# Kernel optimization log

Hardware: AMD Instinct MI355X
Metric: run time of the kernel (lower is better)

The kernel has to match this reference:

```python
import jax, jax.numpy as jnp
import numpy as np

B, N, C = 8192, 64, 256  # batch, num_nodes, cells; depth=2


def setup_inputs() -> dict:
    key = jax.random.key(0)
    ks = jax.random.split(key, 9)
    scale1 = 1.0  # fan_in = 1
    scaleC = 1.0 / np.sqrt(C)
    return {
        "Q": jax.random.normal(ks[0], (B, N), dtype=jnp.float32),
        "Y": jax.random.normal(ks[1], (B, N), dtype=jnp.float32),
        # stacked per-node MLP params: Linear(1,C) -> ReLU -> Linear(C,C) -> ReLU -> Linear(C,1)
        "W1": jax.random.normal(ks[2], (N, 1, C), dtype=jnp.float32) * scale1,
        "b1": jax.random.normal(ks[3], (N, C), dtype=jnp.float32) * scale1,
        "W2": jax.random.normal(ks[4], (N, C, C), dtype=jnp.float32) * scaleC,
        "b2": jax.random.normal(ks[5], (N, C), dtype=jnp.float32) * scaleC,
        "W3": jax.random.normal(ks[6], (N, C, 1), dtype=jnp.float32) * scaleC,
        "b3": jax.random.normal(ks[7], (N, 1), dtype=jnp.float32) * scaleC,
        "bias_0": jnp.ones((1, 1), dtype=jnp.float32),
    }


def reference(Q, Y, W1, b1, W2, b2, W3, b3, bias_0):
    s = Q * Y  # [B, N], per-node scalar input s_i = q_i * y_i
    # layer 1: scalar -> C  (W1[n,0,:] broadcast over batch)
    h = jax.nn.relu(s[:, :, None] * W1[None, :, 0, :] + b1[None])  # [B, N, C]
    # layer 2: C -> C, batched over nodes
    h = jax.nn.relu(jnp.einsum("bnc,ncd->bnd", h, W2) + b2[None])  # [B, N, C]
    # layer 3: C -> scalar
    z_i = jnp.einsum("bnc,nc->bn", h, W3[:, :, 0]) + b3[None, :, 0]  # [B, N]
    z_0 = bias_0 - jnp.sum(s, axis=-1, keepdims=True)  # [B, 1]
    z = jnp.concatenate([z_0, z_i], axis=-1)  # [B, N+1]
    z = jax.nn.softmax(z, axis=-1)
    return jax.nn.relu(z)
```

## Files before the change

### kernel.cpp

```cpp
#include <hip/hip_runtime.h>
#include <hip/hip_bf16.h>


typedef unsigned int u32;

__device__ __forceinline__ float row_reduce16(float x) {
    int v;
    v = __builtin_amdgcn_update_dpp(0, __float_as_int(x), 0xB1, 0xF, 0xF, false);
    x += __int_as_float(v);
    v = __builtin_amdgcn_update_dpp(0, __float_as_int(x), 0x4E, 0xF, 0xF, false);
    x += __int_as_float(v);
    v = __builtin_amdgcn_update_dpp(0, __float_as_int(x), 0x124, 0xF, 0xF, false);
    x += __int_as_float(v);
    v = __builtin_amdgcn_update_dpp(0, __float_as_int(x), 0x128, 0xF, 0xF, false);
    x += __int_as_float(v);
    return x;
}

__global__ __launch_bounds__(256) void prep(
    const float* __restrict__ Q, const float* __restrict__ Y,
    const float* __restrict__ W1, const float* __restrict__ b1,
    float* __restrict__ S, float* __restrict__ knots, int* __restrict__ perm)
{
    __shared__ float ts[64][65];
    __shared__ float key[256];
    __shared__ int   idx[256];

    const int blk = blockIdx.x;
    const int tid = threadIdx.x;

    if (blk < 128) {
        const int b0 = blk << 6;
        #pragma unroll
        for (int jj = 0; jj < 16; jj++) {
            int i = tid + (jj << 8);
            int r = i >> 6, c = i & 63;
            ts[r][c] = Q[(size_t)(b0 + r) * 64 + c] * Y[(size_t)(b0 + r) * 64 + c];
        }
        __syncthreads();
        #pragma unroll
        for (int jj = 0; jj < 16; jj++) {
            int i = tid + (jj << 8);
            int nn = i >> 6, bb = i & 63;
            S[((size_t)nn << 13) + b0 + bb] = ts[bb][nn];
        }
    } else {
        const int n = blk - 128;
        {
            float w = W1[n * 256 + tid];
            float b = b1[n * 256 + tid];
            key[tid] = -b / w;
            idx[tid] = tid;
        }
        __syncthreads();
        for (int k = 2; k <= 256; k <<= 1) {
            for (int j = k >> 1; j > 0; j >>= 1) {
                int p = tid ^ j;
                if (p > tid) {
                    float a = key[tid], c = key[p];
                    bool up = ((tid & k) == 0);
                    if (up ? (a > c) : (a < c)) {
                        int ia = idx[tid];
                        key[tid] = c; idx[tid] = idx[p];
                        key[p] = a; idx[p] = ia;
                    }
                }
                __syncthreads();
            }
        }
        knots[n * 256 + tid] = key[tid];
        perm[n * 256 + tid]  = idx[tid];
    }
}

__global__ __launch_bounds__(256) void build_sort(
    const float* __restrict__ W1, const float* __restrict__ b1,
    const float* __restrict__ W2, const float* __restrict__ b2,
    const float* __restrict__ W3, const int* __restrict__ perm,
    const float* __restrict__ S, const float* __restrict__ knots,
    float4* __restrict__ entries, float2* __restrict__ AccP,
    unsigned char* __restrict__ cnt8, uint2* __restrict__ sorted)
{
    __shared__ float  w1s[256], b1s[256], kns[256];
    __shared__ int    pm[256];
    __shared__ float  part[16][16][8];
    __shared__ float2 accL[257];
    __shared__ u32    hist[257];

    const int blk = blockIdx.x;
    const int tid = threadIdx.x;
    const int lane = tid & 63;

    if (blk < 512) {
        const int n    = blk >> 3;
        const int strip= blk & 7;
        const int prl  = tid & 15;
        const int seg  = tid >> 4;
        const int prg  = (strip << 4) + prl;
        const int d0   = prg << 1;
        const int g    = (n << 3) + strip;

        w1s[tid] = W1[n * 256 + tid];
        b1s[tid] = b1[n * 256 + tid];
        kns[tid] = knots[n * 256 + tid];
        pm[tid]  = perm[n * 256 + tid];
        __syncthreads();

        const float w30 = W3[n * 256 + d0];
        const float w31 = W3[n * 256 + d0 + 1];
        const float* W2n = W2 + ((size_t)n << 16);
        float2 vreg[16];

        {
            float ba0 = 0.f, bc0 = 0.f, ba1 = 0.f, bc1 = 0.f;
            float da0 = 0.f, dc0 = 0.f, da1 = 0.f, dc1 = 0.f;
            #pragma unroll
            for (int i = 0; i < 16; ++i) {
                int   kj = pm[(seg << 4) + i];
                float w  = w1s[kj];
                float bb = b1s[kj];
                float2 v = *reinterpret_cast<const float2*>(&W2n[kj * 256 + d0]);
                vreg[i] = v;
                if (w < 0.f) {
                    ba0 = fmaf(v.x, w, ba0); bc0 = fmaf(v.x, bb, bc0);
                    ba1 = fmaf(v.y, w, ba1); bc1 = fmaf(v.y, bb, bc1);
                }
                float aw = fabsf(w);
                float cs = (w > 0.f) ? bb : -bb;
                da0 = fmaf(v.x, aw, da0); dc0 = fmaf(v.x, cs, dc0);
                da1 = fmaf(v.y, aw, da1); dc1 = fmaf(v.y, cs, dc1);
            }
            float* p = part[seg][prl];
            p[0] = ba0; p[1] = bc0; p[2] = ba1; p[3] = bc1;
            p[4] = da0; p[5] = dc0; p[6] = da1; p[7] = dc1;
        }
        __syncthreads();

        if (tid < 16) {
            const int pr = tid;
            float sa0 = 0.f, sc0 = 0.f, sa1 = 0.f, sc1 = 0.f;
            #pragma unroll
            for (int sg = 0; sg < 16; ++sg) {
                const float* p = part[sg][pr];
                sa0 += p[0]; sc0 += p[1]; sa1 += p[2]; sc1 += p[3];
            }
            const int dd = ((strip << 4) + pr) << 1;
            sc0 += b2[n * 256 + dd];
            sc1 += b2[n * 256 + dd + 1];

            float k0 = kns[0];
            float hLo0 = (sa0 != 0.f) ? -sa0 : sc0;
            float hHi0 = fmaf(sa0, k0, sc0);
            float hLo1 = (sa1 != 0.f) ? -sa1 : sc1;
            float hHi1 = fmaf(sa1, k0, sc1);
            bool act0 = hLo0 > 0.f && hHi0 > 0.f, drp0 = hLo0 <= 0.f && hHi0 <= 0.f;
            bool act1 = hLo1 > 0.f && hHi1 > 0.f, drp1 = hLo1 <= 0.f && hHi1 <= 0.f;
            bool cr0 = !act0 && !drp0, cr1 = !act1 && !drp1;
            float As = (act0 ? w30 * sa0 : 0.f) + (act1 ? w31 * sa1 : 0.f);
            float Bs = (act0 ? w30 * sc0 : 0.f) + (act1 ? w31 * sc1 : 0.f);
            As = row_reduce16(As); Bs = row_reduce16(Bs);
            u32 cx = (u32)cr0 + (u32)cr1;
            u32 incl = cx, t;
            t = __shfl_up(incl, 1, 64); if (pr >= 1) incl += t;
            t = __shfl_up(incl, 2, 64); if (pr >= 2) incl += t;
            t = __shfl_up(incl, 4, 64); if (pr >= 4) incl += t;
            t = __shfl_up(incl, 8, 64); if (pr >= 8) incl += t;
            u32 excl = incl - cx;
            u32 tot  = __shfl(incl, 15, 64);
            size_t eb = ((size_t)(n * 257 + 0) * 8 + strip) * 32;
            u32 off = excl;
            if (cr0) { entries[eb + off] = make_float4(sa0, sc0, w30, 0.f); off++; }
            if (cr1) { entries[eb + off] = make_float4(sa1, sc1, w31, 0.f); }
            if (pr == 0) { accL[0] = make_float2(As, Bs); hist[0] = tot; }

            float ra0 = sa0, rc0 = sc0, ra1 = sa1, rc1 = sc1;
            #pragma unroll
            for (int sg = 0; sg < 16; ++sg) {
                float* p = part[sg][pr];
                float t4 = p[4], t5 = p[5], t6 = p[6], t7 = p[7];
                p[0] = ra0; p[1] = rc0; p[2] = ra1; p[3] = rc1;
                ra0 += t4; rc0 += t5; ra1 += t6; rc1 += t7;
            }
        }
        __syncthreads();

        {
            const float* p = part[seg][prl];
            float a0 = p[0], c0 = p[1], a1 = p[2], c1 = p[3];
            #pragma unroll 4
            for (int i = 0; i < 16; ++i) {
                int   j  = (seg << 4) + i;
                int   kj = pm[j];
                float w  = w1s[kj];
                float bb = b1s[kj];
                float2 v = vreg[i];
                float aw = fabsf(w);
                float cs = (w > 0.f) ? bb : -bb;
                a0 = fmaf(v.x, aw, a0); c0 = fmaf(v.x, cs, c0);
                a1 = fmaf(v.y, aw, a1); c1 = fmaf(v.y, cs, c1);

                float lo = kns[j];
                float hLo0 = fmaf(a0, lo, c0), hLo1 = fmaf(a1, lo, c1);
                float hHi0, hHi1;
                if (j < 255) {
                    float hi = kns[j + 1];
                    hHi0 = fmaf(a0, hi, c0); hHi1 = fmaf(a1, hi, c1);
                } else {
                    hHi0 = (a0 != 0.f) ? a0 : c0;
                    hHi1 = (a1 != 0.f) ? a1 : c1;
                }
                bool act0 = hLo0 > 0.f && hHi0 > 0.f, drp0 = hLo0 <= 0.f && hHi0 <= 0.f;
                bool act1 = hLo1 > 0.f && hHi1 > 0.f, drp1 = hLo1 <= 0.f && hHi1 <= 0.f;
                bool cr0 = !act0 && !drp0, cr1 = !act1 && !drp1;
                float As = (act0 ? w30 * a0 : 0.f) + (act1 ? w31 * a1 : 0.f);
                float Bs = (act0 ? w30 * c0 : 0.f) + (act1 ? w31 * c1 : 0.f);
                As = row_reduce16(As); Bs = row_reduce16(Bs);
                u32 cx = (u32)cr0 + (u32)cr1;
                u32 incl = cx, t;
                t = __shfl_up(incl, 1, 64); if (prl >= 1) incl += t;
                t = __shfl_up(incl, 2, 64); if (prl >= 2) incl += t;
                t = __shfl_up(incl, 4, 64); if (prl >= 4) incl += t;
                t = __shfl_up(incl, 8, 64); if (prl >= 8) incl += t;
                u32 excl = incl - cx;
                u32 tot  = __shfl(incl, (lane & ~15) + 15, 64);
                size_t eb = ((size_t)(n * 257 + (j + 1)) * 8 + strip) * 32;
                u32 off = excl;
                if (cr0) { entries[eb + off] = make_float4(a0, c0, w30, 0.f); off++; }
                if (cr1) { entries[eb + off] = make_float4(a1, c1, w31, 0.f); }
                if (prl == 0) {
                    accL[j + 1] = make_float2(As, Bs);
                    hist[j + 1] = tot;
                }
            }
        }
        __syncthreads();

        for (int i = tid; i < 257; i += 256) {
            AccP[(size_t)g * 257 + i] = accL[i];
            cnt8[(size_t)g * 257 + i] = (unsigned char)hist[i];
        }
    } else {
        const int t = blk - 512;
        const int n = t >> 2;
        const int q = t & 3;

        float* kn = w1s;
        kn[tid] = knots[n * 256 + tid];
        hist[tid] = 0;
        if (tid == 0) hist[256] = 0;
        __syncthreads();

        const float* Sn = S + ((size_t)n << 13) + (q << 11);
        float sv[8]; int iv[8];
        #pragma unroll
        for (int j = 0; j < 8; ++j) {
            const float s = Sn[tid + (j << 8)];
            sv[j] = s;
            int I = 0;
            #pragma unroll
            for (int step = 128; step >= 1; step >>= 1)
                if (kn[I + step - 1] < s) I += step;
            if (I < 256 && kn[I] < s) I += 1;
            iv[j] = I;
            atomicAdd(&hist[I], 1u);
        }
        __syncthreads();

        if (tid < 64) {
            int base = tid << 2;
            u32 h0 = hist[base], h1 = hist[base + 1], h2 = hist[base + 2], h3 = hist[base + 3];
            u32 lsum = h0 + h1 + h2 + h3;
            u32 run = lsum;
            #pragma unroll
            for (int off = 1; off < 64; off <<= 1) {
                u32 tt = __shfl_up(run, off, 64);
                if (lane >= off) run += tt;
            }
            u32 excl = run - lsum;
            hist[base]     = excl;
            hist[base + 1] = excl + h0;
            hist[base + 2] = excl + h0 + h1;
            hist[base + 3] = excl + h0 + h1 + h2;
            if (tid == 63) hist[256] = excl + lsum;
        }
        __syncthreads();

        uint2* dst = sorted + ((size_t)n << 13) + (q << 11);
        #pragma unroll
        for (int j = 0; j < 8; ++j) {
            u32 pos = atomicAdd(&hist[iv[j]], 1u);
            u32 bglob = (u32)((q << 11) + tid + (j << 8));
            dst[pos] = make_uint2(__float_as_uint(sv[j]), ((u32)iv[j] << 13) | bglob);
        }
    }
}

__global__ __launch_bounds__(256) void eval_nodes(
    const uint2* __restrict__ sorted, const float4* __restrict__ entries,
    const float2* __restrict__ AccP, const unsigned char* __restrict__ cnt8,
    const float* __restrict__ b3, float* __restrict__ Z)
{
    const int n   = blockIdx.x;
    const int c0  = blockIdx.y << 8;
    const int tid = threadIdx.x;

    const uint2 ent = sorted[((size_t)n << 13) + c0 + tid];
    const float s   = __uint_as_float(ent.x);
    const int   I   = (int)(ent.y >> 13);
    const int   bl  = (int)(ent.y & 8191u);

    const size_t ibase = (size_t)(n * 257 + I) * 8;

    float A = 0.f, B = 0.f, zc = 0.f;
    #pragma unroll
    for (int st = 0; st < 8; ++st) {
        const size_t gi = (size_t)((n << 3) + st) * 257 + I;
        float2 ap = AccP[gi];
        A += ap.x; B += ap.y;
        u32 c = cnt8[gi];
        const float4* ep = entries + ((ibase + st) << 5);
        for (u32 jj = 0; jj < c; ++jj) {
            float4 e = ep[jj];
            zc = fmaf(e.z, fmaxf(fmaf(e.x, s, e.y), 0.f), zc);
        }
    }
    Z[((size_t)n << 13) + bl] = fmaf(A, s, B) + zc + b3[n];
}

__global__ __launch_bounds__(256) void softmax_rows(
    const float* __restrict__ Q, const float* __restrict__ Y,
    const float* __restrict__ Z, const float* __restrict__ bias0,
    float* __restrict__ out)
{
    __shared__ float ts[64][65];
    const int b0   = blockIdx.x << 6;
    const int tid  = threadIdx.x;
    const int lane = tid & 63;
    const int wv   = tid >> 6;

    #pragma unroll
    for (int jj = 0; jj < 16; jj++) {
        int idx = tid + (jj << 8);
        int nn = idx >> 6, bb = idx & 63;
        ts[bb][nn] = Z[((size_t)nn << 13) + b0 + bb];
    }
    __syncthreads();

    const float bias = bias0[0];
    #pragma unroll 2
    for (int r = 0; r < 16; ++r) {
        const int row = (wv << 4) + r;
        const int b   = b0 + row;

        float s = Q[(size_t)b * 64 + lane] * Y[(size_t)b * 64 + lane];
        float ssum = s;
        #pragma unroll
        for (int mask = 32; mask >= 1; mask >>= 1) ssum += __shfl_xor(ssum, mask, 64);
        const float z0 = bias - ssum;

        float zl = ts[row][lane];
        float mx = zl;
        #pragma unroll
        for (int mask = 32; mask >= 1; mask >>= 1) mx = fmaxf(mx, __shfl_xor(mx, mask, 64));
        mx = fmaxf(mx, z0);

        float el = expf(zl - mx);
        float e0 = expf(z0 - mx);
        float den = el;
        #pragma unroll
        for (int mask = 32; mask >= 1; mask >>= 1) den += __shfl_xor(den, mask, 64);
        den += e0;
        const float inv = 1.0f / den;

        out[(size_t)b * 65 + 1 + lane] = el * inv;
        if (lane == 0) out[(size_t)b * 65] = e0 * inv;
    }
}

extern "C" void kernel_launch(void* const* d_in, const int* in_sizes, int n_in,
                              void* d_out, int out_size, void* d_ws, size_t ws_size,
                              hipStream_t stream)
{
    const float* Q     = (const float*)d_in[0];
    const float* Y     = (const float*)d_in[1];
    const float* W1    = (const float*)d_in[2];
    const float* b1    = (const float*)d_in[3];
    const float* W2    = (const float*)d_in[4];
    const float* b2    = (const float*)d_in[5];
    const float* W3    = (const float*)d_in[6];
    const float* b3    = (const float*)d_in[7];
    const float* bias0 = (const float*)d_in[8];
    float* out = (float*)d_out;

    char* ws = (char*)d_ws;
    float4* entries      = (float4*)ws;
    float2* AccP         = (float2*)(ws + 67371008);
    unsigned char* cnt8  = (unsigned char*)(ws + 68423680);
    float* S             = (float*)(ws + 68555264);
    float* Z             = (float*)(ws + 70652416);
    float* knots         = (float*)(ws + 72749568);
    int*   perm          = (int*)  (ws + 72815104);
    uint2* sorted        = (uint2*)(ws + 72880640);

    prep<<<192, 256, 0, stream>>>(Q, Y, W1, b1, S, knots, perm);
    build_sort<<<768, 256, 0, stream>>>(W1, b1, W2, b2, W3, perm, S, knots,
                                        entries, AccP, cnt8, sorted);
    eval_nodes<<<dim3(64, 32), 256, 0, stream>>>(sorted, entries, AccP, cnt8, b3, Z);
    softmax_rows<<<128, 256, 0, stream>>>(Q, Y, Z, bias0, out);
}
```

Before: 55.71 us.

## Move knot binning and sort into eval_nodes as a per-block LDS sort

The bucket-sort of per-batch scalars by knot interval moves out of the build kernel, where it ran as 256 extra blocks writing a global sorted array, into eval_nodes. Each eval block now does the binary search, histogram, scan and scatter in shared memory over its own 256 samples. This removes the global sorted buffer's write and read traffic and drops the build kernel to 512 blocks. In exchange, sorting happens only within each 256-sample chunk, so lanes in a wave share interval indices less often and the entry loops diverge more; eval_nodes also gains LDS work and syncs.

```diff
diff --git a/kernel.cpp b/kernel.cpp
--- a/kernel.cpp
+++ b/kernel.cpp
@@ -73,248 +73,238 @@
     }
 }
 
-__global__ __launch_bounds__(256) void build_sort(
+__global__ __launch_bounds__(256) void build_scan(
     const float* __restrict__ W1, const float* __restrict__ b1,
     const float* __restrict__ W2, const float* __restrict__ b2,
     const float* __restrict__ W3, const int* __restrict__ perm,
-    const float* __restrict__ S, const float* __restrict__ knots,
+    const float* __restrict__ knots,
     float4* __restrict__ entries, float2* __restrict__ AccP,
-    unsigned char* __restrict__ cnt8, uint2* __restrict__ sorted)
+    unsigned char* __restrict__ cnt8)
 {
     __shared__ float  w1s[256], b1s[256], kns[256];
     __shared__ int    pm[256];
     __shared__ float  part[16][16][8];
     __shared__ float2 accL[257];
-    __shared__ u32    hist[257];
-
-    const int blk = blockIdx.x;
-    const int tid = threadIdx.x;
+    __shared__ u32    cntL[257];
+
+    const int tid  = threadIdx.x;
     const int lane = tid & 63;
-
-    if (blk < 512) {
-        const int n    = blk >> 3;
-        const int strip= blk & 7;
-        const int prl  = tid & 15;
-        const int seg  = tid >> 4;
-        const int prg  = (strip << 4) + prl;
-        const int d0   = prg << 1;
-        const int g    = (n << 3) + strip;
-
-        w1s[tid] = W1[n * 256 + tid];
-        b1s[tid] = b1[n * 256 + tid];
-        kns[tid] = knots[n * 256 + tid];
-        pm[tid]  = perm[n * 256 + tid];
-        __syncthreads();
-
-        const float w30 = W3[n * 256 + d0];
-        const float w31 = W3[n * 256 + d0 + 1];
-        const float* W2n = W2 + ((size_t)n << 16);
-        float2 vreg[16];
-
-        {
-            float ba0 = 0.f, bc0 = 0.f, ba1 = 0.f, bc1 = 0.f;
-            float da0 = 0.f, dc0 = 0.f, da1 = 0.f, dc1 = 0.f;
-            #pragma unroll
-            for (int i = 0; i < 16; ++i) {
-                int   kj = pm[(seg << 4) + i];
-                float w  = w1s[kj];
-                float bb = b1s[kj];
-                float2 v = *reinterpret_cast<const float2*>(&W2n[kj * 256 + d0]);
-                vreg[i] = v;
-                if (w < 0.f) {
-                    ba0 = fmaf(v.x, w, ba0); bc0 = fmaf(v.x, bb, bc0);
-                    ba1 = fmaf(v.y, w, ba1); bc1 = fmaf(v.y, bb, bc1);
-                }
-                float aw = fabsf(w);
-                float cs = (w > 0.f) ? bb : -bb;
-                da0 = fmaf(v.x, aw, da0); dc0 = fmaf(v.x, cs, dc0);
-                da1 = fmaf(v.y, aw, da1); dc1 = fmaf(v.y, cs, dc1);
+    const int n    = blockIdx.x >> 3;
+    const int strip= blockIdx.x & 7;
+    const int prl  = tid & 15;
+    const int seg  = tid >> 4;
+    const int d0   = ((strip << 4) + prl) << 1;
+    const int g    = (n << 3) + strip;
+
+    w1s[tid] = W1[n * 256 + tid];
+    b1s[tid] = b1[n * 256 + tid];
+    kns[tid] = knots[n * 256 + tid];
+    pm[tid]  = perm[n * 256 + tid];
+    __syncthreads();
+
+    const float w30 = W3[n * 256 + d0];
+    const float w31 = W3[n * 256 + d0 + 1];
+    const float* W2n = W2 + ((size_t)n << 16);
+    float2 vreg[16];
+
+    {
+        float ba0 = 0.f, bc0 = 0.f, ba1 = 0.f, bc1 = 0.f;
+        float da0 = 0.f, dc0 = 0.f, da1 = 0.f, dc1 = 0.f;
+        #pragma unroll
+        for (int i = 0; i < 16; ++i) {
+            int   kj = pm[(seg << 4) + i];
+            float w  = w1s[kj];
+            float bb = b1s[kj];
+            float2 v = *reinterpret_cast<const float2*>(&W2n[kj * 256 + d0]);
+            vreg[i] = v;
+            if (w < 0.f) {
+                ba0 = fmaf(v.x, w, ba0); bc0 = fmaf(v.x, bb, bc0);
+                ba1 = fmaf(v.y, w, ba1); bc1 = fmaf(v.y, bb, bc1);
             }
-            float* p = part[seg][prl];
-            p[0] = ba0; p[1] = bc0; p[2] = ba1; p[3] = bc1;
-            p[4] = da0; p[5] = dc0; p[6] = da1; p[7] = dc1;
-        }
-        __syncthreads();
-
-        if (tid < 16) {
-            const int pr = tid;
-            float sa0 = 0.f, sc0 = 0.f, sa1 = 0.f, sc1 = 0.f;
-            #pragma unroll
-            for (int sg = 0; sg < 16; ++sg) {
-                const float* p = part[sg][pr];
-                sa0 += p[0]; sc0 += p[1]; sa1 += p[2]; sc1 += p[3];
+            float aw = fabsf(w);
+            float cs = (w > 0.f) ? bb : -bb;
+            da0 = fmaf(v.x, aw, da0); dc0 = fmaf(v.x, cs, dc0);
+            da1 = fmaf(v.y, aw, da1); dc1 = fmaf(v.y, cs, dc1);
+        }
+        float* p = part[seg][prl];
+        p[0] = ba0; p[1] = bc0; p[2] = ba1; p[3] = bc1;
+        p[4] = da0; p[5] = dc0; p[6] = da1; p[7] = dc1;
+    }
+    __syncthreads();
+
+    if (tid < 16) {
+        const int pr = tid;
+        float sa0 = 0.f, sc0 = 0.f, sa1 = 0.f, sc1 = 0.f;
+        #pragma unroll
+        for (int sg = 0; sg < 16; ++sg) {
+            const float* p = part[sg][pr];
+            sa0 += p[0]; sc0 += p[1]; sa1 += p[2]; sc1 += p[3];
+        }
+        const int dd = ((strip << 4) + pr) << 1;
+        sc0 += b2[n * 256 + dd];
+        sc1 += b2[n * 256 + dd + 1];
+
+        float k0 = kns[0];
+        float hLo0 = (sa0 != 0.f) ? -sa0 : sc0;
+        float hHi0 = fmaf(sa0, k0, sc0);
+        float hLo1 = (sa1 != 0.f) ? -sa1 : sc1;
+        float hHi1 = fmaf(sa1, k0, sc1);
+        bool act0 = hLo0 > 0.f && hHi0 > 0.f, drp0 = hLo0 <= 0.f && hHi0 <= 0.f;
+        bool act1 = hLo1 > 0.f && hHi1 > 0.f, drp1 = hLo1 <= 0.f && hHi1 <= 0.f;
+        bool cr0 = !act0 && !drp0, cr1 = !act1 && !drp1;
+        float As = (act0 ? w30 * sa0 : 0.f) + (act1 ? w31 * sa1 : 0.f);
+        float Bs = (act0 ? w30 * sc0 : 0.f) + (act1 ? w31 * sc1 : 0.f);
+        As = row_reduce16(As); Bs = row_reduce16(Bs);
+        u32 cx = (u32)cr0 + (u32)cr1;
+        u32 incl = cx, t;
+        t = __shfl_up(incl, 1, 64); if (pr >= 1) incl += t;
+        t = __shfl_up(incl, 2, 64); if (pr >= 2) incl += t;
+        t = __shfl_up(incl, 4, 64); if (pr >= 4) incl += t;
+        t = __shfl_up(incl, 8, 64); if (pr >= 8) incl += t;
+        u32 excl = incl - cx;
+        u32 tot  = __shfl(incl, 15, 64);
+        size_t eb = ((size_t)(n * 257 + 0) * 8 + strip) * 32;
+        u32 off = excl;
+        if (cr0) { entries[eb + off] = make_float4(sa0, sc0, w30, 0.f); off++; }
+        if (cr1) { entries[eb + off] = make_float4(sa1, sc1, w31, 0.f); }
+        if (pr == 0) { accL[0] = make_float2(As, Bs); cntL[0] = tot; }
+
+        float ra0 = sa0, rc0 = sc0, ra1 = sa1, rc1 = sc1;
+        #pragma unroll
+        for (int sg = 0; sg < 16; ++sg) {
+            float* p = part[sg][pr];
+            float t4 = p[4], t5 = p[5], t6 = p[6], t7 = p[7];
+            p[0] = ra0; p[1] = rc0; p[2] = ra1; p[3] = rc1;
+            ra0 += t4; rc0 += t5; ra1 += t6; rc1 += t7;
+        }
+    }
+    __syncthreads();
+
+    {
+        const float* p = part[seg][prl];
+        float a0 = p[0], c0 = p[1], a1 = p[2], c1 = p[3];
+        #pragma unroll 4
+        for (int i = 0; i < 16; ++i) {
+            int   j  = (seg << 4) + i;
+            int   kj = pm[j];
+            float w  = w1s[kj];
+            float bb = b1s[kj];
+            float2 v = vreg[i];
+            float aw = fabsf(w);
+            float cs = (w > 0.f) ? bb : -bb;
+            a0 = fmaf(v.x, aw, a0); c0 = fmaf(v.x, cs, c0);
+            a1 = fmaf(v.y, aw, a1); c1 = fmaf(v.y, cs, c1);
+
+            float lo = kns[j];
+            float hLo0 = fmaf(a0, lo, c0), hLo1 = fmaf(a1, lo, c1);
+            float hHi0, hHi1;
+            if (j < 255) {
+                float hi = kns[j + 1];
+                hHi0 = fmaf(a0, hi, c0); hHi1 = fmaf(a1, hi, c1);
+            } else {
+                hHi0 = (a0 != 0.f) ? a0 : c0;
+                hHi1 = (a1 != 0.f) ? a1 : c1;
             }
-            const int dd = ((strip << 4) + pr) << 1;
-            sc0 += b2[n * 256 + dd];
-            sc1 += b2[n * 256 + dd + 1];
-
-            float k0 = kns[0];
-            float hLo0 = (sa0 != 0.f) ? -sa0 : sc0;
-            float hHi0 = fmaf(sa0, k0, sc0);
-            float hLo1 = (sa1 != 0.f) ? -sa1 : sc1;
-            float hHi1 = fmaf(sa1, k0, sc1);
             bool act0 = hLo0 > 0.f && hHi0 > 0.f, drp0 = hLo0 <= 0.f && hHi0 <= 0.f;
             bool act1 = hLo1 > 0.f && hHi1 > 0.f, drp1 = hLo1 <= 0.f && hHi1 <= 0.f;
             bool cr0 = !act0 && !drp0, cr1 = !act1 && !drp1;
-            float As = (act0 ? w30 * sa0 : 0.f) + (act1 ? w31 * sa1 : 0.f);
-            float Bs = (act0 ? w30 * sc0 : 0.f) + (act1 ? w31 * sc1 : 0.f);
+            float As = (act0 ? w30 * a0 : 0.f) + (act1 ? w31 * a1 : 0.f);
+            float Bs = (act0 ? w30 * c0 : 0.f) + (act1 ? w31 * c1 : 0.f);
             As = row_reduce16(As); Bs = row_reduce16(Bs);
             u32 cx = (u32)cr0 + (u32)cr1;
             u32 incl = cx, t;
-            t = __shfl_up(incl, 1, 64); if (pr >= 1) incl += t;
-            t = __shfl_up(incl, 2, 64); if (pr >= 2) incl += t;
-            t = __shfl_up(incl, 4, 64); if (pr >= 4) incl += t;
-            t = __shfl_up(incl, 8, 64); if (pr >= 8) incl += t;
+            t = __shfl_up(incl, 1, 64); if (prl >= 1) incl += t;
+            t = __shfl_up(incl, 2, 64); if (prl >= 2) incl += t;
+            t = __shfl_up(incl, 4, 64); if (prl >= 4) incl += t;
+            t = __shfl_up(incl, 8, 64); if (prl >= 8) incl += t;
             u32 excl = incl - cx;
-            u32 tot  = __shfl(incl, 15, 64);
-            size_t eb = ((size_t)(n * 257 + 0) * 8 + strip) * 32;
+            u32 tot  = __shfl(incl, (lane & ~15) + 15, 64);
+            size_t eb = ((size_t)(n * 257 + (j + 1)) * 8 + strip) * 32;
             u32 off = excl;
-            if (cr0) { entries[eb + off] = make_float4(sa0, sc0, w30, 0.f); off++; }
-            if (cr1) { entries[eb + off] = make_float4(sa1, sc1, w31, 0.f); }
-            if (pr == 0) { accL[0] = make_float2(As, Bs); hist[0] = tot; }
-
-            float ra0 = sa0, rc0 = sc0, ra1 = sa1, rc1 = sc1;
-            #pragma unroll
-            for (int sg = 0; sg < 16; ++sg) {
-                float* p = part[sg][pr];
-                float t4 = p[4], t5 = p[5], t6 = p[6], t7 = p[7];
-                p[0] = ra0; p[1] = rc0; p[2] = ra1; p[3] = rc1;
-                ra0 += t4; rc0 += t5; ra1 += t6; rc1 += t7;
+            if (cr0) { entries[eb + off] = make_float4(a0, c0, w30, 0.f); off++; }
+            if (cr1) { entries[eb + off] = make_float4(a1, c1, w31, 0.f); }
+            if (prl == 0) {
+                accL[j + 1] = make_float2(As, Bs);
+                cntL[j + 1] = tot;
             }
         }
-        __syncthreads();
-
-        {
-            const float* p = part[seg][prl];
-            float a0 = p[0], c0 = p[1], a1 = p[2], c1 = p[3];
-            #pragma unroll 4
-            for (int i = 0; i < 16; ++i) {
-                int   j  = (seg << 4) + i;
-                int   kj = pm[j];
-                float w  = w1s[kj];
-                float bb = b1s[kj];
-                float2 v = vreg[i];
-                float aw = fabsf(w);
-                float cs = (w > 0.f) ? bb : -bb;
-                a0 = fmaf(v.x, aw, a0); c0 = fmaf(v.x, cs, c0);
-                a1 = fmaf(v.y, aw, a1); c1 = fmaf(v.y, cs, c1);
-
-                float lo = kns[j];
-                float hLo0 = fmaf(a0, lo, c0), hLo1 = fmaf(a1, lo, c1);
-                float hHi0, hHi1;
-                if (j < 255) {
-                    float hi = kns[j + 1];
-                    hHi0 = fmaf(a0, hi, c0); hHi1 = fmaf(a1, hi, c1);
-                } else {
-                    hHi0 = (a0 != 0.f) ? a0 : c0;
-                    hHi1 = (a1 != 0.f) ? a1 : c1;
-                }
-                bool act0 = hLo0 > 0.f && hHi0 > 0.f, drp0 = hLo0 <= 0.f && hHi0 <= 0.f;
-                bool act1 = hLo1 > 0.f && hHi1 > 0.f, drp1 = hLo1 <= 0.f && hHi1 <= 0.f;
-                bool cr0 = !act0 && !drp0, cr1 = !act1 && !drp1;
-                float As = (act0 ? w30 * a0 : 0.f) + (act1 ? w31 * a1 : 0.f);
-                float Bs = (act0 ? w30 * c0 : 0.f) + (act1 ? w31 * c1 : 0.f);
-                As = row_reduce16(As); Bs = row_reduce16(Bs);
-                u32 cx = (u32)cr0 + (u32)cr1;
-                u32 incl = cx, t;
-                t = __shfl_up(incl, 1, 64); if (prl >= 1) incl += t;
-                t = __shfl_up(incl, 2, 64); if (prl >= 2) incl += t;
-                t = __shfl_up(incl, 4, 64); if (prl >= 4) incl += t;
-                t = __shfl_up(incl, 8, 64); if (prl >= 8) incl += t;
-                u32 excl = incl - cx;
-                u32 tot  = __shfl(incl, (lane & ~15) + 15, 64);
-                size_t eb = ((size_t)(n * 257 + (j + 1)) * 8 + strip) * 32;
-                u32 off = excl;
-                if (cr0) { entries[eb + off] = make_float4(a0, c0, w30, 0.f); off++; }
-                if (cr1) { entries[eb + off] = make_float4(a1, c1, w31, 0.f); }
-                if (prl == 0) {
-                    accL[j + 1] = make_float2(As, Bs);
-                    hist[j + 1] = tot;
-                }
-            }
-        }
-        __syncthreads();
-
-        for (int i = tid; i < 257; i += 256) {
-            AccP[(size_t)g * 257 + i] = accL[i];
-            cnt8[(size_t)g * 257 + i] = (unsigned char)hist[i];
-        }
-    } else {
-        const int t = blk - 512;
-        const int n = t >> 2;
-        const int q = t & 3;
-
-        float* kn = w1s;
-        kn[tid] = knots[n * 256 + tid];
-        hist[tid] = 0;
-        if (tid == 0) hist[256] = 0;
-        __syncthreads();
-
-        const float* Sn = S + ((size_t)n << 13) + (q << 11);
-        float sv[8]; int iv[8];
-        #pragma unroll
-        for (int j = 0; j < 8; ++j) {
-            const float s = Sn[tid + (j << 8)];
-            sv[j] = s;
-            int I = 0;
-            #pragma unroll
-            for (int step = 128; step >= 1; step >>= 1)
-                if (kn[I + step - 1] < s) I += step;
-            if (I < 256 && kn[I] < s) I += 1;
-            iv[j] = I;
-            atomicAdd(&hist[I], 1u);
-        }
-        __syncthreads();
-
-        if (tid < 64) {
-            int base = tid << 2;
-            u32 h0 = hist[base], h1 = hist[base + 1], h2 = hist[base + 2], h3 = hist[base + 3];
-            u32 lsum = h0 + h1 + h2 + h3;
-            u32 run = lsum;
-            #pragma unroll
-            for (int off = 1; off < 64; off <<= 1) {
-                u32 tt = __shfl_up(run, off, 64);
-                if (lane >= off) run += tt;
-            }
-            u32 excl = run - lsum;
-            hist[base]     = excl;
-            hist[base + 1] = excl + h0;
-            hist[base + 2] = excl + h0 + h1;
-            hist[base + 3] = excl + h0 + h1 + h2;
-            if (tid == 63) hist[256] = excl + lsum;
-        }
-        __syncthreads();
-
-        uint2* dst = sorted + ((size_t)n << 13) + (q << 11);
-        #pragma unroll
-        for (int j = 0; j < 8; ++j) {
-            u32 pos = atomicAdd(&hist[iv[j]], 1u);
-            u32 bglob = (u32)((q << 11) + tid + (j << 8));
-            dst[pos] = make_uint2(__float_as_uint(sv[j]), ((u32)iv[j] << 13) | bglob);
-        }
+    }
+    __syncthreads();
+
+    for (int i = tid; i < 257; i += 256) {
+        AccP[(size_t)g * 257 + i] = accL[i];
+        cnt8[(size_t)g * 257 + i] = (unsigned char)cntL[i];
     }
 }
 
 __global__ __launch_bounds__(256) void eval_nodes(
-    const uint2* __restrict__ sorted, const float4* __restrict__ entries,
-    const float2* __restrict__ AccP, const unsigned char* __restrict__ cnt8,
-    const float* __restrict__ b3, float* __restrict__ Z)
-{
+    const float* __restrict__ S, const float* __restrict__ knots,
+    const float4* __restrict__ entries, const float2* __restrict__ AccP,
+    const unsigned char* __restrict__ cnt8, const float* __restrict__ b3,
+    float* __restrict__ Z)
+{
+    __shared__ float kn[256];
+    __shared__ float ssv[256];
+    __shared__ u32   meta[256];
+    __shared__ u32   hist[257];
+
     const int n   = blockIdx.x;
     const int c0  = blockIdx.y << 8;
     const int tid = threadIdx.x;
-
-    const uint2 ent = sorted[((size_t)n << 13) + c0 + tid];
-    const float s   = __uint_as_float(ent.x);
-    const int   I   = (int)(ent.y >> 13);
-    const int   bl  = (int)(ent.y & 8191u);
-
-    const size_t ibase = (size_t)(n * 257 + I) * 8;
+    const int lane = tid & 63;
+
+    kn[tid] = knots[n * 256 + tid];
+    hist[tid] = 0;
+    if (tid == 0) hist[256] = 0;
+
+    const float sv = S[((size_t)n << 13) + c0 + tid];
+    __syncthreads();
+
+    int I = 0;
+    #pragma unroll
+    for (int step = 128; step >= 1; step >>= 1)
+        if (kn[I + step - 1] < sv) I += step;
+    if (I < 256 && kn[I] < sv) I += 1;
+    atomicAdd(&hist[I], 1u);
+    __syncthreads();
+
+    if (tid < 64) {
+        int base = tid << 2;
+        u32 h0 = hist[base], h1 = hist[base + 1], h2 = hist[base + 2], h3 = hist[base + 3];
+        u32 lsum = h0 + h1 + h2 + h3;
+        u32 run = lsum;
+        #pragma unroll
+        for (int off = 1; off < 64; off <<= 1) {
+            u32 tt = __shfl_up(run, off, 64);
+            if (lane >= off) run += tt;
+        }
+        u32 excl = run - lsum;
+        hist[base]     = excl;
+        hist[base + 1] = excl + h0;
+        hist[base + 2] = excl + h0 + h1;
+        hist[base + 3] = excl + h0 + h1 + h2;
+        if (tid == 63) hist[256] = excl + lsum;
+    }
+    __syncthreads();
+
+    {
+        u32 pos = atomicAdd(&hist[I], 1u);
+        ssv[pos]  = sv;
+        meta[pos] = ((u32)I << 8) | (u32)tid;
+    }
+    __syncthreads();
+
+    const float s = ssv[tid];
+    const u32   m = meta[tid];
+    const int   Iv = (int)(m >> 8);
+    const int   bl = c0 + (int)(m & 255u);
+
+    const size_t ibase = (size_t)(n * 257 + Iv) * 8;
 
     float A = 0.f, B = 0.f, zc = 0.f;
     #pragma unroll
     for (int st = 0; st < 8; ++st) {
-        const size_t gi = (size_t)((n << 3) + st) * 257 + I;
+        const size_t gi = (size_t)((n << 3) + st) * 257 + Iv;
         float2 ap = AccP[gi];
         A += ap.x; B += ap.y;
         u32 c = cnt8[gi];
@@ -400,11 +390,10 @@
     float* Z             = (float*)(ws + 70652416);
     float* knots         = (float*)(ws + 72749568);
     int*   perm          = (int*)  (ws + 72815104);
-    uint2* sorted        = (uint2*)(ws + 72880640);
 
     prep<<<192, 256, 0, stream>>>(Q, Y, W1, b1, S, knots, perm);
-    build_sort<<<768, 256, 0, stream>>>(W1, b1, W2, b2, W3, perm, S, knots,
-                                        entries, AccP, cnt8, sorted);
-    eval_nodes<<<dim3(64, 32), 256, 0, stream>>>(sorted, entries, AccP, cnt8, b3, Z);
+    build_scan<<<512, 256, 0, stream>>>(W1, b1, W2, b2, W3, perm, knots,
+                                        entries, AccP, cnt8);
+    eval_nodes<<<dim3(64, 32), 256, 0, stream>>>(S, knots, entries, AccP, cnt8, b3, Z);
     softmax_rows<<<128, 256, 0, stream>>>(Q, Y, Z, bias0, out);
 }
```

Measured after the change: 56.48 us. No clear change (+1.4%).
